# Kernel tuning notes

Hardware: AMD Instinct MI355X
Metric: run time of the kernel (lower is better)

Reference implementation:

```python
import jax, jax.numpy as jnp
import numpy as np

E = 4          # num_experts
B = 32         # batch
CIN = 64
COUT = 64
H = 112
WID = 112
K = 3          # kernel size


def setup_inputs() -> dict:
    key = jax.random.key(0)
    k1, k2, k3, k4 = jax.random.split(key, 4)
    x = jax.random.normal(k1, (B, CIN, H, WID), dtype=jnp.float32)
    layer_mask = jax.random.uniform(k2, (B, E), dtype=jnp.float32)
    # per-expert conv weights/biases (kaiming-ish scale)
    W = jax.random.normal(k3, (E, COUT, CIN, K, K), dtype=jnp.float32) * 0.05
    b = jax.random.normal(k4, (E, COUT), dtype=jnp.float32) * 0.05
    return {"x": x, "layer_mask": layer_mask, "W": W, "b": b}


def _conv(x, w):
    # stride 1, padding 1 on both spatial dims (matches nn.Conv2d(k=3, s=1, p=1))
    return jax.lax.conv_general_dilated(
        x, w, window_strides=(1, 1), padding=[(1, 1), (1, 1)],
        dimension_numbers=("NCHW", "OIHW", "NCHW"))


def reference(x, layer_mask, W, b):
    # Loop over the small fixed expert set, accumulating the gated sum to
    # avoid materializing an [E, B, C, H, W] intermediate.
    out = jnp.zeros((B, COUT, H, WID), dtype=x.dtype)
    for e in range(E):
        expert_out = _conv(x, W[e]) + b[e][None, :, None, None]
        gate = layer_mask[:, e][:, None, None, None]  # [B,1,1,1]
        out = out + expert_out * gate
    return out
```

## Files before the change

### kernel.cpp

```cpp
#include <hip/hip_runtime.h>
#include <stdint.h>

#define CIN   64
#define COUT  64
#define HH    112
#define WW    112
#define NEXP  4
#define HW    (HH * WW)

typedef short bf16x8 __attribute__((ext_vector_type(8)));
typedef float f32x16 __attribute__((ext_vector_type(16)));

__device__ inline uint16_t f2bf(float f) {
    uint32_t u = __builtin_bit_cast(uint32_t, f);
    return (uint16_t)((u + 0x7FFFu + ((u >> 16) & 1u)) >> 16);
}

__device__ __forceinline__ void gll16(const uint16_t* g, uint16_t* l) {
    __builtin_amdgcn_global_load_lds(
        (const __attribute__((address_space(1))) uint32_t*)g,
        (__attribute__((address_space(3))) uint32_t*)l, 16, 0, 0);
}

__global__ __launch_bounds__(256)
void xform_x(const float* __restrict__ x, uint16_t* __restrict__ Xt) {
    __shared__ float lds[CIN][WW + 1];
    const int hp = blockIdx.x % 114;
    const int n  = blockIdx.x / 114;
    const int h  = hp - 1;
    uint16_t* orow = Xt + ((size_t)(n * 114 + hp)) * 114 * 64;

    if (h < 0 || h >= HH) {
        const uint4 z = {0, 0, 0, 0};
        for (int u = threadIdx.x; u < 114 * 8; u += 256)
            *(uint4*)(orow + u * 8) = z;
        return;
    }
    for (int i = threadIdx.x; i < CIN * WW; i += 256) {
        int ci = i / WW, w = i % WW;
        lds[ci][w] = x[((size_t)(n * CIN + ci)) * HW + h * WW + w];
    }
    __syncthreads();
    for (int u = threadIdx.x; u < 114 * 8; u += 256) {
        int wp = u >> 3, cg = u & 7;
        int w = wp - 1;
        union { uint16_t s[8]; uint4 v; } pk;
        if (w < 0 || w >= WW) {
            pk.v = (uint4){0, 0, 0, 0};
        } else {
#pragma unroll
            for (int j = 0; j < 8; ++j) pk.s[j] = f2bf(lds[cg * 8 + j][w]);
        }
        *(uint4*)(orow + (size_t)u * 8) = pk.v;
    }
}

__global__ __launch_bounds__(256)
void fold_wb(const float* __restrict__ W, const float* __restrict__ bias,
             const float* __restrict__ mask,
             uint16_t* __restrict__ Weff, float* __restrict__ Beff, int B) {
    int idx = blockIdx.x * 256 + threadIdx.x;
    if (idx >= B * 72 * 512) return;
    int j   = idx & 7;
    int co  = (idx >> 3) & 63;
    int g   = (idx >> 9) % 72;
    int n   = idx / (512 * 72);
    int par   = g & 1;
    int kq    = (g >> 1) & 1;
    int khw   = (g >> 2) % 9;
    int phase = (g >> 2) / 9;
    int ci = phase * 32 + (kq * 2 + par) * 8 + j;
    float acc = 0.f;
#pragma unroll
    for (int e = 0; e < NEXP; ++e)
        acc = fmaf(mask[n * NEXP + e],
                   W[((size_t)(e * COUT + co) * CIN + ci) * 9 + khw], acc);
    Weff[idx] = f2bf(acc);
    if (g == 0 && j == 0) {
        float ba = 0.f;
#pragma unroll
        for (int e = 0; e < NEXP; ++e)
            ba = fmaf(mask[n * NEXP + e], bias[e * COUT + co], ba);
        Beff[n * COUT + co] = ba;
    }
}

__device__ inline void compute_phase(const uint16_t* __restrict__ buf,
                                     const uint16_t* __restrict__ wp,
                                     int rowb, int colb, int par,
                                     f32x16& acc00, f32x16& acc01,
                                     f32x16& acc10, f32x16& acc11) {
#pragma unroll 3
    for (int khw = 0; khw < 9; ++khw) {
        const int dh = khw / 3;
        const int dw = khw - dh * 3;
        const int pb0 = (rowb + dh) * 18 + (colb + dw);
        const int pb1 = pb0 + 36;
        const int f0 = (pb0 >> 1) & 3, f1 = (pb1 >> 1) & 3;
        const uint16_t* lp0 = &buf[pb0 * 32];
        const uint16_t* lp1 = &buf[pb1 * 32];
#pragma unroll
        for (int kq = 0; kq < 2; ++kq) {
            const int cgA = kq * 2 + par;
            bf16x8 b0 = *(const bf16x8*)(lp0 + ((cgA ^ f0) << 3));
            bf16x8 b1 = *(const bf16x8*)(lp1 + ((cgA ^ f1) << 3));
            const uint16_t* wk = wp + (size_t)((khw * 2 + kq) * 2) * 512;
            bf16x8 a0 = *(const bf16x8*)(wk);
            bf16x8 a1 = *(const bf16x8*)(wk + 256);
            acc00 = __builtin_amdgcn_mfma_f32_32x32x16_bf16(a0, b0, acc00, 0, 0, 0);
            acc01 = __builtin_amdgcn_mfma_f32_32x32x16_bf16(a0, b1, acc01, 0, 0, 0);
            acc10 = __builtin_amdgcn_mfma_f32_32x32x16_bf16(a1, b0, acc10, 0, 0, 0);
            acc11 = __builtin_amdgcn_mfma_f32_32x32x16_bf16(a1, b1, acc11, 0, 0, 0);
        }
    }
}

__global__ __launch_bounds__(256, 3)
void conv_gll(const uint16_t* __restrict__ Xt, const uint16_t* __restrict__ Weff,
              const float* __restrict__ Beff, float* __restrict__ out,
              int nwg) {
    __shared__ uint16_t ldsx[2592 * 8];

    int bid = blockIdx.x;
    if ((nwg & 7) == 0)
        bid = (bid & 7) * (nwg >> 3) + (bid >> 3);

    const int tid  = threadIdx.x;
    const int lane = tid & 63;
    const int wid  = tid >> 6;
    const int tileIdx = bid % 49;
    const int n  = bid / 49;
    const int th = tileIdx / 7, tw = tileIdx % 7;
    const int h0 = th * 16, w0 = tw * 16;

    const uint16_t* xt_n = Xt + (size_t)n * (114 * 114 * 64);

#pragma unroll
    for (int it = 0; it < 10; ++it) {
        int u  = it * 256 + tid;
        int ph = (u >= 1296) ? 1 : 0;
        int v  = u - ph * 1296;
        int pix = v >> 2, s = v & 3;
        int dh = pix / 18, dw = pix - dh * 18;
        int cg = s ^ ((pix >> 1) & 3);
        const uint16_t* src = xt_n + ((size_t)(h0 + dh) * 114 + (w0 + dw)) * 64
                            + ph * 32 + cg * 8;
        uint16_t* dst = ldsx + (size_t)(it * 256 + wid * 64) * 8;
        gll16(src, dst);
    }
    if (tid < 32) {
        int v = 1264 + tid;
        int pix = v >> 2, s = v & 3;
        int dh = pix / 18, dw = pix - dh * 18;
        int cg = s ^ ((pix >> 1) & 3);
        const uint16_t* src = xt_n + ((size_t)(h0 + dh) * 114 + (w0 + dw)) * 64
                            + 32 + cg * 8;
        *(uint4*)(ldsx + (size_t)(2560 + tid) * 8) = *(const uint4*)src;
    }
    __syncthreads();

    const int rowb = wid * 4 + ((lane & 31) >> 4);
    const int colb = lane & 15;
    const int par  = lane >> 5;

    const uint16_t* wbase = Weff + (size_t)n * 36864
                          + (size_t)par * 512 + (size_t)(lane & 31) * 8;

    f32x16 acc00 = {}, acc01 = {}, acc10 = {}, acc11 = {};
    compute_phase(ldsx,         wbase,                rowb, colb, par,
                  acc00, acc01, acc10, acc11);
    compute_phase(ldsx + 10368, wbase + 36 * 512,     rowb, colb, par,
                  acc00, acc01, acc10, acc11);

    const float* bptr = Beff + n * 64;
    const int row0 = h0 + rowb;
    const int col  = w0 + colb;
#pragma unroll
    for (int r = 0; r < 16; ++r) {
        const int co = (r & 3) + 8 * (r >> 2) + 4 * par;
        const float bia0 = bptr[co];
        const float bia1 = bptr[co + 32];
        size_t o00 = ((size_t)(n * COUT + co) * HH + row0) * WW + col;
        __builtin_nontemporal_store(acc00[r] + bia0, &out[o00]);
        __builtin_nontemporal_store(acc01[r] + bia0, &out[o00 + 2 * WW]);
        size_t o10 = o00 + (size_t)32 * HW;
        __builtin_nontemporal_store(acc10[r] + bia1, &out[o10]);
        __builtin_nontemporal_store(acc11[r] + bia1, &out[o10 + 2 * WW]);
    }
}

#define COB   8
#define PIX_PER_BLK 256
#define NTILE (HW / PIX_PER_BLK)

__global__ void fold_weights(const float* __restrict__ W,
                             const float* __restrict__ mask,
                             float* __restrict__ Weff, int B) {
    int idx = blockIdx.x * blockDim.x + threadIdx.x;
    int total = B * CIN * 9 * COUT;
    if (idx >= total) return;
    int co = idx % COUT;
    int t  = idx / COUT;
    int k  = t % 9;
    t /= 9;
    int ci = t % CIN;
    int n  = t / CIN;
    float acc = 0.f;
#pragma unroll
    for (int e = 0; e < NEXP; ++e)
        acc = fmaf(mask[n * NEXP + e],
                   W[(((size_t)(e * COUT + co) * CIN + ci) * 9) + k], acc);
    Weff[idx] = acc;
}

__global__ __launch_bounds__(PIX_PER_BLK, 4)
void conv_gated(const float* __restrict__ x,
                const float* __restrict__ mask,
                const float* __restrict__ bias,
                const float* __restrict__ Weff,
                float* __restrict__ out) {
    const int tile = blockIdx.x % NTILE;
    const int cob  = (blockIdx.x / NTILE) % (COUT / COB);
    const int n    = blockIdx.x / (NTILE * (COUT / COB));
    const int p = tile * PIX_PER_BLK + threadIdx.x;
    const int h = p / WW;
    const int w = p % WW;
    const int co0 = cob * COB;

    float acc[COB];
#pragma unroll
    for (int j = 0; j < COB; ++j) {
        float a = 0.f;
#pragma unroll
        for (int e = 0; e < NEXP; ++e)
            a = fmaf(mask[n * NEXP + e], bias[e * COUT + co0 + j], a);
        acc[j] = a;
    }

    const float* xb = x + (((size_t)n * CIN) * HH + h) * WW + w;
    const float* wb = Weff + ((size_t)n * CIN) * 9 * COUT + co0;
    const bool rok0 = (h > 0), rok2 = (h < HH - 1);
    const bool cok0 = (w > 0), cok2 = (w < WW - 1);

    for (int ci = 0; ci < CIN; ++ci) {
        const float* xc = xb + (size_t)ci * HW;
        const float* wc = wb + (size_t)ci * 9 * COUT;
#pragma unroll
        for (int kh = 0; kh < 3; ++kh) {
            const bool rok = (kh == 0) ? rok0 : ((kh == 2) ? rok2 : true);
#pragma unroll
            for (int kw = 0; kw < 3; ++kw) {
                const bool cok = (kw == 0) ? cok0 : ((kw == 2) ? cok2 : true);
                float xv = (rok && cok) ? xc[(kh - 1) * WW + (kw - 1)] : 0.f;
                const float4* wk = (const float4*)(wc + (kh * 3 + kw) * COUT);
                float4 wa = wk[0], wb4 = wk[1];
                acc[0] = fmaf(xv, wa.x, acc[0]);
                acc[1] = fmaf(xv, wa.y, acc[1]);
                acc[2] = fmaf(xv, wa.z, acc[2]);
                acc[3] = fmaf(xv, wa.w, acc[3]);
                acc[4] = fmaf(xv, wb4.x, acc[4]);
                acc[5] = fmaf(xv, wb4.y, acc[5]);
                acc[6] = fmaf(xv, wb4.z, acc[6]);
                acc[7] = fmaf(xv, wb4.w, acc[7]);
            }
        }
    }
    float* ob = out + (((size_t)(n * COUT + co0)) * HH + h) * WW + w;
#pragma unroll
    for (int j = 0; j < COB; ++j)
        ob[(size_t)j * HW] = acc[j];
}

extern "C" void kernel_launch(void* const* d_in, const int* in_sizes, int n_in,
                              void* d_out, int out_size, void* d_ws, size_t ws_size,
                              hipStream_t stream) {
    const float* x    = (const float*)d_in[0];
    const float* mask = (const float*)d_in[1];
    const float* W    = (const float*)d_in[2];
    const float* b    = (const float*)d_in[3];
    float* out = (float*)d_out;

    const int B = in_sizes[0] / (CIN * HW);
    const size_t weffB = (size_t)B * 36864 * 2;
    const size_t beffB = (size_t)B * COUT * 4;
    const size_t xtB   = (size_t)B * 114 * 114 * 64 * 2;
    const size_t need  = weffB + beffB + xtB;

    if (ws_size >= need) {
        uint16_t* Weff = (uint16_t*)d_ws;
        float*    Beff = (float*)((char*)d_ws + weffB);
        uint16_t* Xt   = (uint16_t*)((char*)d_ws + weffB + beffB);
        int foldBlocks = (B * 72 * 512 + 255) / 256;
        fold_wb<<<foldBlocks, 256, 0, stream>>>(W, b, mask, Weff, Beff, B);
        xform_x<<<B * 114, 256, 0, stream>>>(x, Xt);
        const int nwg = B * 49;
        conv_gll<<<nwg, 256, 0, stream>>>(Xt, Weff, Beff, out, nwg);
    } else {
        float* Weff = (float*)d_ws;
        const size_t weff_elems = (size_t)B * CIN * 9 * COUT;
        int foldBlocks = (int)((weff_elems + 255) / 256);
        fold_weights<<<foldBlocks, 256, 0, stream>>>(W, mask, Weff, B);
        conv_gated<<<B * (COUT / COB) * NTILE, PIX_PER_BLK, 0, stream>>>(
            x, mask, b, Weff, out);
    }
}
```

Baseline: 93.13 us.

## Merge prep kernels and halve conv LDS by loading channel phases sequentially

Fuses the weight-folding and input-transform kernels into one launch, with block index ranges choosing the role, which removes one kernel launch and its gap. In the conv kernel the LDS tile now holds only one 32-channel phase at a time and is reloaded between phases behind a barrier, halving shared memory per workgroup so more workgroups can fit per CU. The cost is that the second phase's global-to-LDS load is no longer issued up front, which adds an extra barrier and exposed load latency mid-kernel.

```diff
diff --git a/kernel.cpp b/kernel.cpp
--- a/kernel.cpp
+++ b/kernel.cpp
@@ -23,65 +23,66 @@
 }
 
 __global__ __launch_bounds__(256)
-void xform_x(const float* __restrict__ x, uint16_t* __restrict__ Xt) {
-    __shared__ float lds[CIN][WW + 1];
-    const int hp = blockIdx.x % 114;
-    const int n  = blockIdx.x / 114;
-    const int h  = hp - 1;
-    uint16_t* orow = Xt + ((size_t)(n * 114 + hp)) * 114 * 64;
-
-    if (h < 0 || h >= HH) {
-        const uint4 z = {0, 0, 0, 0};
-        for (int u = threadIdx.x; u < 114 * 8; u += 256)
-            *(uint4*)(orow + u * 8) = z;
-        return;
-    }
-    for (int i = threadIdx.x; i < CIN * WW; i += 256) {
-        int ci = i / WW, w = i % WW;
-        lds[ci][w] = x[((size_t)(n * CIN + ci)) * HW + h * WW + w];
-    }
-    __syncthreads();
-    for (int u = threadIdx.x; u < 114 * 8; u += 256) {
-        int wp = u >> 3, cg = u & 7;
-        int w = wp - 1;
-        union { uint16_t s[8]; uint4 v; } pk;
-        if (w < 0 || w >= WW) {
-            pk.v = (uint4){0, 0, 0, 0};
-        } else {
-#pragma unroll
-            for (int j = 0; j < 8; ++j) pk.s[j] = f2bf(lds[cg * 8 + j][w]);
-        }
-        *(uint4*)(orow + (size_t)u * 8) = pk.v;
-    }
-}
-
-__global__ __launch_bounds__(256)
-void fold_wb(const float* __restrict__ W, const float* __restrict__ bias,
-             const float* __restrict__ mask,
-             uint16_t* __restrict__ Weff, float* __restrict__ Beff, int B) {
-    int idx = blockIdx.x * 256 + threadIdx.x;
-    if (idx >= B * 72 * 512) return;
-    int j   = idx & 7;
-    int co  = (idx >> 3) & 63;
-    int g   = (idx >> 9) % 72;
-    int n   = idx / (512 * 72);
-    int par   = g & 1;
-    int kq    = (g >> 1) & 1;
-    int khw   = (g >> 2) % 9;
-    int phase = (g >> 2) / 9;
-    int ci = phase * 32 + (kq * 2 + par) * 8 + j;
-    float acc = 0.f;
-#pragma unroll
-    for (int e = 0; e < NEXP; ++e)
-        acc = fmaf(mask[n * NEXP + e],
-                   W[((size_t)(e * COUT + co) * CIN + ci) * 9 + khw], acc);
-    Weff[idx] = f2bf(acc);
-    if (g == 0 && j == 0) {
-        float ba = 0.f;
+void prep(const float* __restrict__ x, const float* __restrict__ W,
+          const float* __restrict__ bias, const float* __restrict__ mask,
+          uint16_t* __restrict__ Xt, uint16_t* __restrict__ Weff,
+          float* __restrict__ Beff, int B) {
+    const int nxf = B * 114;
+    if ((int)blockIdx.x < nxf) {
+        __shared__ float lds[CIN][WW + 1];
+        const int hp = blockIdx.x % 114;
+        const int n  = blockIdx.x / 114;
+        const int h  = hp - 1;
+        uint16_t* orow = Xt + ((size_t)(n * 114 + hp)) * 114 * 64;
+
+        if (h < 0 || h >= HH) {
+            const uint4 z = {0, 0, 0, 0};
+            for (int u = threadIdx.x; u < 114 * 8; u += 256)
+                *(uint4*)(orow + u * 8) = z;
+            return;
+        }
+        for (int i = threadIdx.x; i < CIN * WW; i += 256) {
+            int ci = i / WW, w = i % WW;
+            lds[ci][w] = x[((size_t)(n * CIN + ci)) * HW + h * WW + w];
+        }
+        __syncthreads();
+        for (int u = threadIdx.x; u < 114 * 8; u += 256) {
+            int wp = u >> 3, cg = u & 7;
+            int w = wp - 1;
+            union { uint16_t s[8]; uint4 v; } pk;
+            if (w < 0 || w >= WW) {
+                pk.v = (uint4){0, 0, 0, 0};
+            } else {
+#pragma unroll
+                for (int j = 0; j < 8; ++j) pk.s[j] = f2bf(lds[cg * 8 + j][w]);
+            }
+            *(uint4*)(orow + (size_t)u * 8) = pk.v;
+        }
+    } else {
+        int idx = (blockIdx.x - nxf) * 256 + threadIdx.x;
+        if (idx >= B * 72 * 512) return;
+        int j   = idx & 7;
+        int co  = (idx >> 3) & 63;
+        int g   = (idx >> 9) % 72;
+        int n   = idx / (512 * 72);
+        int par   = g & 1;
+        int kq    = (g >> 1) & 1;
+        int khw   = (g >> 2) % 9;
+        int phase = (g >> 2) / 9;
+        int ci = phase * 32 + (kq * 2 + par) * 8 + j;
+        float acc = 0.f;
 #pragma unroll
         for (int e = 0; e < NEXP; ++e)
-            ba = fmaf(mask[n * NEXP + e], bias[e * COUT + co], ba);
-        Beff[n * COUT + co] = ba;
+            acc = fmaf(mask[n * NEXP + e],
+                       W[((size_t)(e * COUT + co) * CIN + ci) * 9 + khw], acc);
+        Weff[idx] = f2bf(acc);
+        if (g == 0 && j == 0) {
+            float ba = 0.f;
+#pragma unroll
+            for (int e = 0; e < NEXP; ++e)
+                ba = fmaf(mask[n * NEXP + e], bias[e * COUT + co], ba);
+            Beff[n * COUT + co] = ba;
+        }
     }
 }
 
@@ -119,7 +120,7 @@
 void conv_gll(const uint16_t* __restrict__ Xt, const uint16_t* __restrict__ Weff,
               const float* __restrict__ Beff, float* __restrict__ out,
               int nwg) {
-    __shared__ uint16_t ldsx[2592 * 8];
+    __shared__ uint16_t ldsx[1296 * 8];
 
     int bid = blockIdx.x;
     if ((nwg & 7) == 0)
@@ -135,30 +136,6 @@
 
     const uint16_t* xt_n = Xt + (size_t)n * (114 * 114 * 64);
 
-#pragma unroll
-    for (int it = 0; it < 10; ++it) {
-        int u  = it * 256 + tid;
-        int ph = (u >= 1296) ? 1 : 0;
-        int v  = u - ph * 1296;
-        int pix = v >> 2, s = v & 3;
-        int dh = pix / 18, dw = pix - dh * 18;
-        int cg = s ^ ((pix >> 1) & 3);
-        const uint16_t* src = xt_n + ((size_t)(h0 + dh) * 114 + (w0 + dw)) * 64
-                            + ph * 32 + cg * 8;
-        uint16_t* dst = ldsx + (size_t)(it * 256 + wid * 64) * 8;
-        gll16(src, dst);
-    }
-    if (tid < 32) {
-        int v = 1264 + tid;
-        int pix = v >> 2, s = v & 3;
-        int dh = pix / 18, dw = pix - dh * 18;
-        int cg = s ^ ((pix >> 1) & 3);
-        const uint16_t* src = xt_n + ((size_t)(h0 + dh) * 114 + (w0 + dw)) * 64
-                            + 32 + cg * 8;
-        *(uint4*)(ldsx + (size_t)(2560 + tid) * 8) = *(const uint4*)src;
-    }
-    __syncthreads();
-
     const int rowb = wid * 4 + ((lane & 31) >> 4);
     const int colb = lane & 15;
     const int par  = lane >> 5;
@@ -167,10 +144,35 @@
                           + (size_t)par * 512 + (size_t)(lane & 31) * 8;
 
     f32x16 acc00 = {}, acc01 = {}, acc10 = {}, acc11 = {};
-    compute_phase(ldsx,         wbase,                rowb, colb, par,
-                  acc00, acc01, acc10, acc11);
-    compute_phase(ldsx + 10368, wbase + 36 * 512,     rowb, colb, par,
-                  acc00, acc01, acc10, acc11);
+
+#pragma unroll
+    for (int phase = 0; phase < 2; ++phase) {
+        if (phase) __syncthreads();
+#pragma unroll
+        for (int it = 0; it < 5; ++it) {
+            int v  = it * 256 + tid;
+            int pix = v >> 2, s = v & 3;
+            int dh = pix / 18, dw = pix - dh * 18;
+            int cg = s ^ ((pix >> 1) & 3);
+            const uint16_t* src = xt_n
+                + ((size_t)(h0 + dh) * 114 + (w0 + dw)) * 64 + phase * 32 + cg * 8;
+            uint16_t* dst = ldsx + (size_t)(it * 256 + wid * 64) * 8;
+            gll16(src, dst);
+        }
+        if (tid < 16) {
+            int v = 1280 + tid;
+            int pix = v >> 2, s = v & 3;
+            int dh = pix / 18, dw = pix - dh * 18;
+            int cg = s ^ ((pix >> 1) & 3);
+            const uint16_t* src = xt_n
+                + ((size_t)(h0 + dh) * 114 + (w0 + dw)) * 64 + phase * 32 + cg * 8;
+            *(uint4*)(ldsx + (size_t)v * 8) = *(const uint4*)src;
+        }
+        __syncthreads();
+
+        compute_phase(ldsx, wbase + (size_t)phase * 36 * 512,
+                      rowb, colb, par, acc00, acc01, acc10, acc11);
+    }
 
     const float* bptr = Beff + n * 64;
     const int row0 = h0 + rowb;
@@ -291,8 +293,8 @@
         float*    Beff = (float*)((char*)d_ws + weffB);
         uint16_t* Xt   = (uint16_t*)((char*)d_ws + weffB + beffB);
         int foldBlocks = (B * 72 * 512 + 255) / 256;
-        fold_wb<<<foldBlocks, 256, 0, stream>>>(W, b, mask, Weff, Beff, B);
-        xform_x<<<B * 114, 256, 0, stream>>>(x, Xt);
+        prep<<<B * 114 + foldBlocks, 256, 0, stream>>>(x, W, b, mask,
+                                                       Xt, Weff, Beff, B);
         const int nwg = B * 49;
         conv_gll<<<nwg, 256, 0, stream>>>(Xt, Weff, Beff, out, nwg);
     } else {
```

After: 82.63 us. 1.13x faster.
